# Performance work log

Measured on AMD Instinct MI355X. Metric: run time of the kernel, lower is better.

The kernel has to match this reference:

```python
import jax, jax.numpy as jnp
import numpy as np

B, T, CH, Hs, Ws = 2, 64, 512, 24, 24
DIM = CH // 2          # 256, attention channel dim
HEADS = 8
HEAD_DIM = DIM // HEADS  # 32
MAX_SEQ = 64


def setup_inputs() -> dict:
    key = jax.random.key(0)
    ks = jax.random.split(key, 6)
    return {
        "x": jax.random.normal(ks[0], (B, T, CH, Hs, Ws), dtype=jnp.float32),
        "rpb_table": jax.random.normal(ks[1], (2 * MAX_SEQ - 1, HEADS), dtype=jnp.float32) * 0.02,
        "qkv_w": jax.random.normal(ks[2], (3 * DIM, DIM), dtype=jnp.float32) * 0.02,
        "qkv_b": jax.random.normal(ks[3], (3 * DIM,), dtype=jnp.float32) * 0.02,
        "proj_w": jax.random.normal(ks[4], (DIM, DIM), dtype=jnp.float32) * 0.02,
        "proj_b": jax.random.normal(ks[5], (DIM,), dtype=jnp.float32) * 0.02,
    }


def reference(x, rpb_table, qkv_w, qkv_b, proj_w, proj_b):
    b, t, c, h, w = x.shape
    half = c // 2
    a_part = x[:, :, :half]       # (B,T,half,H,W) untouched branch
    b_part = x[:, :, half:]       # attention branch

    # 'b t c h w -> (b h w) t c'
    xb = jnp.transpose(b_part, (0, 3, 4, 1, 2)).reshape(b * h * w, t, half)
    B_, N, C = xb.shape
    scale = HEAD_DIM ** -0.5

    qkv = xb @ qkv_w.T + qkv_b                        # (B_, N, 3*C)
    qkv = qkv.reshape(B_, N, 3, HEADS, HEAD_DIM)
    qkv = jnp.transpose(qkv, (2, 0, 3, 1, 4))          # (3, B_, heads, N, hd)
    q, k, v = qkv[0] * scale, qkv[1], qkv[2]

    attn = jnp.einsum('bhnd,bhmd->bhnm', q, k)         # (B_, heads, N, N)

    # relative position bias: index = p2 - p1 + (MAX_SEQ - 1)
    pos = jnp.arange(t)
    rel_idx = pos[None, :] - pos[:, None] + (MAX_SEQ - 1)   # (N, N)
    bias = rpb_table[rel_idx]                              # (N, N, heads)
    bias = jnp.transpose(bias, (2, 0, 1))                  # (heads, N, N)
    attn = attn + bias[None]

    # causal (mask_future=True): -inf strictly above the diagonal
    causal = jnp.where(pos[None, :] > pos[:, None], -jnp.inf, 0.0).astype(attn.dtype)
    attn = attn + causal[None, None]

    attn = jax.nn.softmax(attn, axis=-1)

    out = jnp.einsum('bhnm,bhmd->bhnd', attn, v)       # (B_, heads, N, hd)
    out = jnp.transpose(out, (0, 2, 1, 3)).reshape(B_, N, C)
    out = out @ proj_w.T + proj_b

    # '(b h w) t c -> b t c h w'
    out = out.reshape(b, h, w, t, half)
    out = jnp.transpose(out, (0, 3, 4, 1, 2))

    return jnp.concatenate([a_part, out], axis=2)
```

## Files before the change

### kernel.cpp

```cpp
#include <hip/hip_runtime.h>
#include <hip/hip_bf16.h>

typedef __attribute__((ext_vector_type(4))) float  f32x4;
typedef __attribute__((ext_vector_type(8))) short  bf16x8;
typedef __attribute__((ext_vector_type(8))) unsigned short u16x8;
typedef __attribute__((ext_vector_type(4))) unsigned short u16x4;

__device__ __forceinline__ unsigned short f2bf(float f) {
    union { float f; unsigned u; } v; v.f = f;
    unsigned u = v.u;
    unsigned r = u + 0x7fffu + ((u >> 16) & 1u);
    return (unsigned short)(r >> 16);
}

__device__ __forceinline__ void gload16(const void* g, void* l) {
    __builtin_amdgcn_global_load_lds((const __attribute__((address_space(1))) unsigned*)g,
                                     (__attribute__((address_space(3))) unsigned*)l, 16, 0, 0);
}


__global__ void cvt_weights(const float* __restrict__ qkv_w, const float* __restrict__ proj_w,
                            unsigned short* __restrict__ wq, unsigned short* __restrict__ wp) {
    int i = blockIdx.x * 256 + threadIdx.x;
    if (i < 196608) wq[i] = f2bf(qkv_w[i]);
    else            wp[i - 196608] = f2bf(proj_w[i - 196608]);
}

__global__ void copy_a(const float* __restrict__ x, float* __restrict__ out) {
    long long i = (long long)blockIdx.x * 256 + threadIdx.x;
    int chunk = (int)(i / 36864);
    int r     = (int)(i % 36864);
    size_t off = (size_t)chunk * 73728 + r;
    ((float4*)out)[off] = ((const float4*)x)[off];
}

__global__ __launch_bounds__(256) void transpose_b(const float* __restrict__ x,
                                                   unsigned short* __restrict__ xb) {
    __shared__ unsigned short tile[256][72];
    const int bt  = blockIdx.x;
    const int hw0 = blockIdx.y * 64;
    const int tid = threadIdx.x;
    const float* src = x + ((size_t)bt * 512 + 256) * 576 + hw0;
    const int c_sub = tid >> 4, l16 = tid & 15;
    #pragma unroll
    for (int it = 0; it < 16; ++it) {
        int cc = it * 16 + c_sub;
        const float4 v = *(const float4*)(src + (size_t)cc * 576 + l16 * 4);
        tile[cc][l16 * 4 + 0] = f2bf(v.x);
        tile[cc][l16 * 4 + 1] = f2bf(v.y);
        tile[cc][l16 * 4 + 2] = f2bf(v.z);
        tile[cc][l16 * 4 + 3] = f2bf(v.w);
    }
    __syncthreads();
    const int row = tid >> 2;
    const int cs  = (tid & 3) * 64;
    const int b = bt >> 6, t = bt & 63;
    size_t m = (size_t)t * 1152 + (size_t)b * 576 + hw0 + row;
    unsigned short* dst = xb + m * 256 + cs;
    #pragma unroll
    for (int q = 0; q < 8; ++q) {
        u16x8 v;
        #pragma unroll
        for (int u = 0; u < 8; ++u) v[u] = tile[cs + q * 8 + u][row];
        *(u16x8*)(dst + q * 8) = v;
    }
}

__global__ __launch_bounds__(256, 4) void gemm_qkv(const unsigned short* __restrict__ A,
                                                   const unsigned short* __restrict__ Wt,
                                                   const float* __restrict__ bias,
                                                   unsigned short* __restrict__ out) {
    __shared__ unsigned short Ws[128 * 64];
    __shared__ unsigned short Xs[128 * 64];
    const int m0 = blockIdx.x * 128, n0 = blockIdx.y * 128;
    const int tid = threadIdx.x;
    const int lane = tid & 63, w = tid >> 6;
    const int wy = w >> 1, wx = w & 1;
    const int c = lane & 15, g = lane >> 4;
    const int lr = lane >> 3, lu = lane & 7;
    const int su = lu ^ lr;
    const int cs7 = c & 7;
    f32x4 acc[4][4] = {};
    for (int k0 = 0; k0 < 256; k0 += 64) {
        #pragma unroll
        for (int q = 0; q < 4; ++q) {
            int R = w * 32 + q * 8;
            gload16(Wt + (size_t)(n0 + R + lr) * 256 + k0 + su * 8, &Ws[R * 64]);
            gload16(A  + (size_t)(m0 + R + lr) * 256 + k0 + su * 8, &Xs[R * 64]);
        }
        __syncthreads();
        #pragma unroll
        for (int kk = 0; kk < 2; ++kk) {
            bf16x8 af[4], bx[4];
            #pragma unroll
            for (int a2 = 0; a2 < 4; ++a2)
                af[a2] = *(const bf16x8*)(&Ws[(wy * 64 + a2 * 16 + c) * 64 + (((kk * 4 + g) ^ cs7) * 8)]);
            #pragma unroll
            for (int b2 = 0; b2 < 4; ++b2)
                bx[b2] = *(const bf16x8*)(&Xs[(wx * 64 + b2 * 16 + c) * 64 + (((kk * 4 + g) ^ cs7) * 8)]);
            #pragma unroll
            for (int a2 = 0; a2 < 4; ++a2)
                #pragma unroll
                for (int b2 = 0; b2 < 4; ++b2)
                    acc[a2][b2] = __builtin_amdgcn_mfma_f32_16x16x32_bf16(af[a2], bx[b2], acc[a2][b2], 0, 0, 0);
        }
        __syncthreads();
    }
    #pragma unroll
    for (int a2 = 0; a2 < 4; ++a2) {
        int n = n0 + wy * 64 + a2 * 16 + g * 4;
        float4 bv = *(const float4*)(bias + n);
        #pragma unroll
        for (int b2 = 0; b2 < 4; ++b2) {
            int m = m0 + wx * 64 + b2 * 16 + c;
            u16x4 v;
            v[0] = f2bf(acc[a2][b2][0] + bv.x);
            v[1] = f2bf(acc[a2][b2][1] + bv.y);
            v[2] = f2bf(acc[a2][b2][2] + bv.z);
            v[3] = f2bf(acc[a2][b2][3] + bv.w);
            *(u16x4*)(out + (size_t)m * 768 + n) = v;
        }
    }
}

__global__ __launch_bounds__(64) void attn_kernel(const unsigned short* __restrict__ qkv,
                                                  const float* __restrict__ rpb,
                                                  unsigned short* __restrict__ att) {
    __shared__ float bias_s[127];
    __shared__ unsigned short vT[32][72];
    __shared__ unsigned short P[64][72];
    const int blk = blockIdx.x;
    const int p = blk >> 3, h = blk & 7;
    const int lane = threadIdx.x;
    const int c = lane & 15, g = lane >> 4;

    bias_s[lane] = rpb[lane * 8 + h];
    if (lane < 63) bias_s[64 + lane] = rpb[(64 + lane) * 8 + h];

    {
        const unsigned short* vrow = qkv + (size_t)(lane * 1152 + p) * 768 + 512 + h * 32;
        #pragma unroll
        for (int q = 0; q < 4; ++q) {
            u16x8 v = *(const u16x8*)(vrow + q * 8);
            #pragma unroll
            for (int u = 0; u < 8; ++u) vT[q * 8 + u][lane] = v[u];
        }
    }
    bf16x8 qf[4], kf[4];
    #pragma unroll
    for (int mt = 0; mt < 4; ++mt)
        qf[mt] = *(const bf16x8*)(qkv + (size_t)((mt * 16 + c) * 1152 + p) * 768 + h * 32 + g * 8);
    #pragma unroll
    for (int nt = 0; nt < 4; ++nt)
        kf[nt] = *(const bf16x8*)(qkv + (size_t)((nt * 16 + c) * 1152 + p) * 768 + 256 + h * 32 + g * 8);
    f32x4 s[4][4] = {};
    #pragma unroll
    for (int mt = 0; mt < 4; ++mt)
        #pragma unroll
        for (int nt = 0; nt < 4; ++nt)
            s[mt][nt] = __builtin_amdgcn_mfma_f32_16x16x32_bf16(qf[mt], kf[nt], s[mt][nt], 0, 0, 0);
    __syncthreads();

    const float scale = 0.17677669529663687f;
    #pragma unroll
    for (int mt = 0; mt < 4; ++mt) {
        #pragma unroll
        for (int r = 0; r < 4; ++r) {
            int i = mt * 16 + g * 4 + r;
            float vals[4];
            #pragma unroll
            for (int nt = 0; nt < 4; ++nt) {
                int j = nt * 16 + c;
                float v = s[mt][nt][r] * scale + bias_s[j - i + 63];
                vals[nt] = (j > i) ? -1e30f : v;
            }
            float mx = fmaxf(fmaxf(vals[0], vals[1]), fmaxf(vals[2], vals[3]));
            #pragma unroll
            for (int off = 1; off < 16; off <<= 1) mx = fmaxf(mx, __shfl_xor(mx, off, 64));
            float sum = 0.f;
            #pragma unroll
            for (int nt = 0; nt < 4; ++nt) { vals[nt] = __expf(vals[nt] - mx); sum += vals[nt]; }
            #pragma unroll
            for (int off = 1; off < 16; off <<= 1) sum += __shfl_xor(sum, off, 64);
            float inv = 1.0f / sum;
            #pragma unroll
            for (int nt = 0; nt < 4; ++nt) P[i][nt * 16 + c] = f2bf(vals[nt] * inv);
        }
    }
    __syncthreads();

    f32x4 o[4][2] = {};
    #pragma unroll
    for (int kk = 0; kk < 2; ++kk) {
        bf16x8 pa[4], vb[2];
        #pragma unroll
        for (int mt = 0; mt < 4; ++mt)
            pa[mt] = *(const bf16x8*)(&P[mt * 16 + c][kk * 32 + g * 8]);
        #pragma unroll
        for (int nt = 0; nt < 2; ++nt)
            vb[nt] = *(const bf16x8*)(&vT[nt * 16 + c][kk * 32 + g * 8]);
        #pragma unroll
        for (int mt = 0; mt < 4; ++mt)
            #pragma unroll
            for (int nt = 0; nt < 2; ++nt)
                o[mt][nt] = __builtin_amdgcn_mfma_f32_16x16x32_bf16(pa[mt], vb[nt], o[mt][nt], 0, 0, 0);
    }
    #pragma unroll
    for (int mt = 0; mt < 4; ++mt)
        #pragma unroll
        for (int nt = 0; nt < 2; ++nt) {
            int d = nt * 16 + c;
            #pragma unroll
            for (int r = 0; r < 4; ++r) {
                int i = mt * 16 + g * 4 + r;
                att[(size_t)(i * 1152 + p) * 256 + h * 32 + d] = f2bf(o[mt][nt][r]);
            }
        }
}

__global__ __launch_bounds__(256, 4) void gemm_proj(const unsigned short* __restrict__ A,
                                                    const unsigned short* __restrict__ Wt,
                                                    const float* __restrict__ bias,
                                                    float* __restrict__ out) {
    __shared__ unsigned short Ws[128 * 64];
    __shared__ unsigned short Xs[128 * 64];
    const int m0 = blockIdx.x * 128, n0 = blockIdx.y * 128;
    const int tid = threadIdx.x;
    const int lane = tid & 63, w = tid >> 6;
    const int wy = w >> 1, wx = w & 1;
    const int c = lane & 15, g = lane >> 4;
    const int lr = lane >> 3, lu = lane & 7;
    const int su = lu ^ lr;
    const int cs7 = c & 7;
    f32x4 acc[4][4] = {};
    for (int k0 = 0; k0 < 256; k0 += 64) {
        #pragma unroll
        for (int q = 0; q < 4; ++q) {
            int R = w * 32 + q * 8;
            gload16(Wt + (size_t)(n0 + R + lr) * 256 + k0 + su * 8, &Ws[R * 64]);
            gload16(A  + (size_t)(m0 + R + lr) * 256 + k0 + su * 8, &Xs[R * 64]);
        }
        __syncthreads();
        #pragma unroll
        for (int kk = 0; kk < 2; ++kk) {
            bf16x8 af[4], bx[4];
            #pragma unroll
            for (int a2 = 0; a2 < 4; ++a2)
                af[a2] = *(const bf16x8*)(&Ws[(wy * 64 + a2 * 16 + c) * 64 + (((kk * 4 + g) ^ cs7) * 8)]);
            #pragma unroll
            for (int b2 = 0; b2 < 4; ++b2)
                bx[b2] = *(const bf16x8*)(&Xs[(wx * 64 + b2 * 16 + c) * 64 + (((kk * 4 + g) ^ cs7) * 8)]);
            #pragma unroll
            for (int a2 = 0; a2 < 4; ++a2)
                #pragma unroll
                for (int b2 = 0; b2 < 4; ++b2)
                    acc[a2][b2] = __builtin_amdgcn_mfma_f32_16x16x32_bf16(af[a2], bx[b2], acc[a2][b2], 0, 0, 0);
        }
        __syncthreads();
    }
    #pragma unroll
    for (int a2 = 0; a2 < 4; ++a2) {
        int n = n0 + wy * 64 + a2 * 16 + g * 4;
        float4 bv = *(const float4*)(bias + n);
        #pragma unroll
        for (int b2 = 0; b2 < 4; ++b2) {
            int m = m0 + wx * 64 + b2 * 16 + c;
            int t   = m / 1152;
            int rem = m % 1152;
            int bb  = rem / 576;
            int hw  = rem % 576;
            float* dst = out + ((size_t)(bb * 64 + t) * 512 + 256 + n) * 576 + hw;
            dst[0]        = acc[a2][b2][0] + bv.x;
            dst[576]      = acc[a2][b2][1] + bv.y;
            dst[2 * 576]  = acc[a2][b2][2] + bv.z;
            dst[3 * 576]  = acc[a2][b2][3] + bv.w;
        }
    }
}

extern "C" void kernel_launch(void* const* d_in, const int* in_sizes, int n_in,
                              void* d_out, int out_size, void* d_ws, size_t ws_size,
                              hipStream_t stream) {
    (void)in_sizes; (void)n_in; (void)out_size;
    const float* x      = (const float*)d_in[0];
    const float* rpb    = (const float*)d_in[1];
    const float* qkv_w  = (const float*)d_in[2];
    const float* qkv_b  = (const float*)d_in[3];
    const float* proj_w = (const float*)d_in[4];
    const float* proj_b = (const float*)d_in[5];
    float* out = (float*)d_out;

    char* ws = (char*)d_ws;
    unsigned short* wq  = (unsigned short*)ws;
    unsigned short* wp  = (unsigned short*)(ws + 393216);
    unsigned short* xb  = (unsigned short*)(ws + 524288);
    unsigned short* qkv = (unsigned short*)(ws + 524288 + 37748736);
    unsigned short* att = xb;
    if (ws_size < (size_t)524288 + 37748736 + 113246208) return;

    cvt_weights<<<1024, 256, 0, stream>>>(qkv_w, proj_w, wq, wp);
    copy_a<<<18432, 256, 0, stream>>>(x, out);
    transpose_b<<<dim3(128, 9), 256, 0, stream>>>(x, xb);
    gemm_qkv<<<dim3(576, 6), 256, 0, stream>>>(xb, wq, qkv_b, qkv);
    attn_kernel<<<9216, 64, 0, stream>>>(qkv, rpb, att);
    gemm_proj<<<dim3(576, 2), 256, 0, stream>>>(att, wp, proj_b, out);
}
```

Baseline: 225.8 us.

## Fuse QKV GEMM, attention, and projection into one per-sequence kernel

Measured after the change: 275.0 us. 21.8% more time.

```diff
diff --git a/kernel.cpp b/kernel.cpp
--- a/kernel.cpp
+++ b/kernel.cpp
@@ -55,7 +55,7 @@
     const int row = tid >> 2;
     const int cs  = (tid & 3) * 64;
     const int b = bt >> 6, t = bt & 63;
-    size_t m = (size_t)t * 1152 + (size_t)b * 576 + hw0 + row;
+    size_t m = ((size_t)(b * 576 + hw0 + row)) * 64 + t;
     unsigned short* dst = xb + m * 256 + cs;
     #pragma unroll
     for (int q = 0; q < 8; ++q) {
@@ -66,102 +66,103 @@
     }
 }
 
-__global__ __launch_bounds__(256, 4) void gemm_qkv(const unsigned short* __restrict__ A,
-                                                   const unsigned short* __restrict__ Wt,
-                                                   const float* __restrict__ bias,
-                                                   unsigned short* __restrict__ out) {
-    __shared__ unsigned short Ws[128 * 64];
-    __shared__ unsigned short Xs[128 * 64];
-    const int m0 = blockIdx.x * 128, n0 = blockIdx.y * 128;
-    const int tid = threadIdx.x;
+__global__ __launch_bounds__(512, 2) void fused_block(
+    const unsigned short* __restrict__ xb,
+    const unsigned short* __restrict__ wqkv,
+    const unsigned short* __restrict__ wproj,
+    const float* __restrict__ qkv_b,
+    const float* __restrict__ proj_b,
+    const float* __restrict__ rpb,
+    float* __restrict__ out)
+{
+    __shared__ unsigned short xs[16384];
+    __shared__ unsigned short wbuf[8][7424];
+    __shared__ float bias_s[1016];
+
+    const int tid  = threadIdx.x;
     const int lane = tid & 63, w = tid >> 6;
-    const int wy = w >> 1, wx = w & 1;
     const int c = lane & 15, g = lane >> 4;
-    const int lr = lane >> 3, lu = lane & 7;
-    const int su = lu ^ lr;
-    const int cs7 = c & 7;
-    f32x4 acc[4][4] = {};
-    for (int k0 = 0; k0 < 256; k0 += 64) {
-        #pragma unroll
-        for (int q = 0; q < 4; ++q) {
-            int R = w * 32 + q * 8;
-            gload16(Wt + (size_t)(n0 + R + lr) * 256 + k0 + su * 8, &Ws[R * 64]);
-            gload16(A  + (size_t)(m0 + R + lr) * 256 + k0 + su * 8, &Xs[R * 64]);
-        }
-        __syncthreads();
-        #pragma unroll
-        for (int kk = 0; kk < 2; ++kk) {
-            bf16x8 af[4], bx[4];
-            #pragma unroll
-            for (int a2 = 0; a2 < 4; ++a2)
-                af[a2] = *(const bf16x8*)(&Ws[(wy * 64 + a2 * 16 + c) * 64 + (((kk * 4 + g) ^ cs7) * 8)]);
+    const int c7 = c & 7;
+    const int bid = blockIdx.x;
+    const int p  = (bid & 7) * 144 + (bid >> 3);
+    const int b  = p / 576, hw = p % 576;
+
+    const unsigned short* src = xb + (size_t)p * 16384;
+    #pragma unroll
+    for (int it = 0; it < 4; ++it) {
+        int U = it * 512 + tid;
+        int r = U >> 5, u = U & 31;
+        gload16(src + r * 256 + ((u ^ (r & 7)) << 3), &xs[U << 3]);
+    }
+    if (tid < 1016) bias_s[tid] = rpb[tid];
+    __syncthreads();
+
+    unsigned short* Q  = &wbuf[w][0];
+    unsigned short* Kl = &wbuf[w][2560];
+    unsigned short* Vt = &wbuf[w][5120];
+    unsigned short* P  = &wbuf[w][0];
+
+    {
+        f32x4 acc[3][2][4] = {};
+        #pragma unroll
+        for (int ks = 0; ks < 8; ++ks) {
+            bf16x8 bx[4];
             #pragma unroll
             for (int b2 = 0; b2 < 4; ++b2)
-                bx[b2] = *(const bf16x8*)(&Xs[(wx * 64 + b2 * 16 + c) * 64 + (((kk * 4 + g) ^ cs7) * 8)]);
-            #pragma unroll
-            for (int a2 = 0; a2 < 4; ++a2)
+                bx[b2] = *(const bf16x8*)(&xs[(b2 * 16 + c) * 256 + (((ks * 4 + g) ^ c7) << 3)]);
+            #pragma unroll
+            for (int mat = 0; mat < 3; ++mat) {
+                bf16x8 af[2];
                 #pragma unroll
-                for (int b2 = 0; b2 < 4; ++b2)
-                    acc[a2][b2] = __builtin_amdgcn_mfma_f32_16x16x32_bf16(af[a2], bx[b2], acc[a2][b2], 0, 0, 0);
-        }
-        __syncthreads();
-    }
-    #pragma unroll
-    for (int a2 = 0; a2 < 4; ++a2) {
-        int n = n0 + wy * 64 + a2 * 16 + g * 4;
-        float4 bv = *(const float4*)(bias + n);
-        #pragma unroll
-        for (int b2 = 0; b2 < 4; ++b2) {
-            int m = m0 + wx * 64 + b2 * 16 + c;
-            u16x4 v;
-            v[0] = f2bf(acc[a2][b2][0] + bv.x);
-            v[1] = f2bf(acc[a2][b2][1] + bv.y);
-            v[2] = f2bf(acc[a2][b2][2] + bv.z);
-            v[3] = f2bf(acc[a2][b2][3] + bv.w);
-            *(u16x4*)(out + (size_t)m * 768 + n) = v;
-        }
-    }
-}
-
-__global__ __launch_bounds__(64) void attn_kernel(const unsigned short* __restrict__ qkv,
-                                                  const float* __restrict__ rpb,
-                                                  unsigned short* __restrict__ att) {
-    __shared__ float bias_s[127];
-    __shared__ unsigned short vT[32][72];
-    __shared__ unsigned short P[64][72];
-    const int blk = blockIdx.x;
-    const int p = blk >> 3, h = blk & 7;
-    const int lane = threadIdx.x;
-    const int c = lane & 15, g = lane >> 4;
-
-    bias_s[lane] = rpb[lane * 8 + h];
-    if (lane < 63) bias_s[64 + lane] = rpb[(64 + lane) * 8 + h];
-
-    {
-        const unsigned short* vrow = qkv + (size_t)(lane * 1152 + p) * 768 + 512 + h * 32;
-        #pragma unroll
-        for (int q = 0; q < 4; ++q) {
-            u16x8 v = *(const u16x8*)(vrow + q * 8);
-            #pragma unroll
-            for (int u = 0; u < 8; ++u) vT[q * 8 + u][lane] = v[u];
-        }
-    }
+                for (int a2 = 0; a2 < 2; ++a2)
+                    af[a2] = *(const bf16x8*)(wqkv + (size_t)(mat * 256 + w * 32 + a2 * 16 + c) * 256 + ks * 32 + g * 8);
+                #pragma unroll
+                for (int a2 = 0; a2 < 2; ++a2)
+                    #pragma unroll
+                    for (int b2 = 0; b2 < 4; ++b2)
+                        acc[mat][a2][b2] = __builtin_amdgcn_mfma_f32_16x16x32_bf16(af[a2], bx[b2], acc[mat][a2][b2], 0, 0, 0);
+            }
+        }
+        const float scale = 0.17677669529663687f;
+        #pragma unroll
+        for (int a2 = 0; a2 < 2; ++a2) {
+            float4 bq = *(const float4*)(qkv_b +       w * 32 + a2 * 16 + g * 4);
+            float4 bk = *(const float4*)(qkv_b + 256 + w * 32 + a2 * 16 + g * 4);
+            float4 bv = *(const float4*)(qkv_b + 512 + w * 32 + a2 * 16 + g * 4);
+            #pragma unroll
+            for (int b2 = 0; b2 < 4; ++b2) {
+                int t = b2 * 16 + c;
+                u16x4 vq, vk;
+                vq[0] = f2bf((acc[0][a2][b2][0] + bq.x) * scale);
+                vq[1] = f2bf((acc[0][a2][b2][1] + bq.y) * scale);
+                vq[2] = f2bf((acc[0][a2][b2][2] + bq.z) * scale);
+                vq[3] = f2bf((acc[0][a2][b2][3] + bq.w) * scale);
+                *(u16x4*)(&Q[t * 40 + a2 * 16 + g * 4]) = vq;
+                vk[0] = f2bf(acc[1][a2][b2][0] + bk.x);
+                vk[1] = f2bf(acc[1][a2][b2][1] + bk.y);
+                vk[2] = f2bf(acc[1][a2][b2][2] + bk.z);
+                vk[3] = f2bf(acc[1][a2][b2][3] + bk.w);
+                *(u16x4*)(&Kl[t * 40 + a2 * 16 + g * 4]) = vk;
+                Vt[(a2 * 16 + g * 4 + 0) * 72 + t] = f2bf(acc[2][a2][b2][0] + bv.x);
+                Vt[(a2 * 16 + g * 4 + 1) * 72 + t] = f2bf(acc[2][a2][b2][1] + bv.y);
+                Vt[(a2 * 16 + g * 4 + 2) * 72 + t] = f2bf(acc[2][a2][b2][2] + bv.z);
+                Vt[(a2 * 16 + g * 4 + 3) * 72 + t] = f2bf(acc[2][a2][b2][3] + bv.w);
+            }
+        }
+    }
+
     bf16x8 qf[4], kf[4];
     #pragma unroll
+    for (int mt = 0; mt < 4; ++mt) qf[mt] = *(const bf16x8*)(&Q[(mt * 16 + c) * 40 + g * 8]);
+    #pragma unroll
+    for (int nt = 0; nt < 4; ++nt) kf[nt] = *(const bf16x8*)(&Kl[(nt * 16 + c) * 40 + g * 8]);
+    f32x4 S[4][4] = {};
+    #pragma unroll
     for (int mt = 0; mt < 4; ++mt)
-        qf[mt] = *(const bf16x8*)(qkv + (size_t)((mt * 16 + c) * 1152 + p) * 768 + h * 32 + g * 8);
-    #pragma unroll
-    for (int nt = 0; nt < 4; ++nt)
-        kf[nt] = *(const bf16x8*)(qkv + (size_t)((nt * 16 + c) * 1152 + p) * 768 + 256 + h * 32 + g * 8);
-    f32x4 s[4][4] = {};
-    #pragma unroll
-    for (int mt = 0; mt < 4; ++mt)
         #pragma unroll
         for (int nt = 0; nt < 4; ++nt)
-            s[mt][nt] = __builtin_amdgcn_mfma_f32_16x16x32_bf16(qf[mt], kf[nt], s[mt][nt], 0, 0, 0);
-    __syncthreads();
-
-    const float scale = 0.17677669529663687f;
+            S[mt][nt] = __builtin_amdgcn_mfma_f32_16x16x32_bf16(qf[mt], kf[nt], S[mt][nt], 0, 0, 0);
+
     #pragma unroll
     for (int mt = 0; mt < 4; ++mt) {
         #pragma unroll
@@ -171,7 +172,7 @@
             #pragma unroll
             for (int nt = 0; nt < 4; ++nt) {
                 int j = nt * 16 + c;
-                float v = s[mt][nt][r] * scale + bias_s[j - i + 63];
+                float v = S[mt][nt][r] + bias_s[(j - i + 63) * 8 + w];
                 vals[nt] = (j > i) ? -1e30f : v;
             }
             float mx = fmaxf(fmaxf(vals[0], vals[1]), fmaxf(vals[2], vals[3]));
@@ -184,96 +185,68 @@
             for (int off = 1; off < 16; off <<= 1) sum += __shfl_xor(sum, off, 64);
             float inv = 1.0f / sum;
             #pragma unroll
-            for (int nt = 0; nt < 4; ++nt) P[i][nt * 16 + c] = f2bf(vals[nt] * inv);
-        }
-    }
-    __syncthreads();
-
-    f32x4 o[4][2] = {};
+            for (int nt = 0; nt < 4; ++nt) P[i * 72 + nt * 16 + c] = f2bf(vals[nt] * inv);
+        }
+    }
+
+    f32x4 O[4][2] = {};
     #pragma unroll
     for (int kk = 0; kk < 2; ++kk) {
         bf16x8 pa[4], vb[2];
         #pragma unroll
         for (int mt = 0; mt < 4; ++mt)
-            pa[mt] = *(const bf16x8*)(&P[mt * 16 + c][kk * 32 + g * 8]);
+            pa[mt] = *(const bf16x8*)(&P[(mt * 16 + c) * 72 + kk * 32 + g * 8]);
         #pragma unroll
         for (int nt = 0; nt < 2; ++nt)
-            vb[nt] = *(const bf16x8*)(&vT[nt * 16 + c][kk * 32 + g * 8]);
+            vb[nt] = *(const bf16x8*)(&Vt[(nt * 16 + c) * 72 + kk * 32 + g * 8]);
         #pragma unroll
         for (int mt = 0; mt < 4; ++mt)
             #pragma unroll
             for (int nt = 0; nt < 2; ++nt)
-                o[mt][nt] = __builtin_amdgcn_mfma_f32_16x16x32_bf16(pa[mt], vb[nt], o[mt][nt], 0, 0, 0);
-    }
+                O[mt][nt] = __builtin_amdgcn_mfma_f32_16x16x32_bf16(pa[mt], vb[nt], O[mt][nt], 0, 0, 0);
+    }
+
+    __syncthreads();
     #pragma unroll
     for (int mt = 0; mt < 4; ++mt)
         #pragma unroll
-        for (int nt = 0; nt < 2; ++nt) {
-            int d = nt * 16 + c;
+        for (int nt = 0; nt < 2; ++nt)
             #pragma unroll
             for (int r = 0; r < 4; ++r) {
-                int i = mt * 16 + g * 4 + r;
-                att[(size_t)(i * 1152 + p) * 256 + h * 32 + d] = f2bf(o[mt][nt][r]);
-            }
-        }
-}
-
-__global__ __launch_bounds__(256, 4) void gemm_proj(const unsigned short* __restrict__ A,
-                                                    const unsigned short* __restrict__ Wt,
-                                                    const float* __restrict__ bias,
-                                                    float* __restrict__ out) {
-    __shared__ unsigned short Ws[128 * 64];
-    __shared__ unsigned short Xs[128 * 64];
-    const int m0 = blockIdx.x * 128, n0 = blockIdx.y * 128;
-    const int tid = threadIdx.x;
-    const int lane = tid & 63, w = tid >> 6;
-    const int wy = w >> 1, wx = w & 1;
-    const int c = lane & 15, g = lane >> 4;
-    const int lr = lane >> 3, lu = lane & 7;
-    const int su = lu ^ lr;
-    const int cs7 = c & 7;
-    f32x4 acc[4][4] = {};
-    for (int k0 = 0; k0 < 256; k0 += 64) {
-        #pragma unroll
-        for (int q = 0; q < 4; ++q) {
-            int R = w * 32 + q * 8;
-            gload16(Wt + (size_t)(n0 + R + lr) * 256 + k0 + su * 8, &Ws[R * 64]);
-            gload16(A  + (size_t)(m0 + R + lr) * 256 + k0 + su * 8, &Xs[R * 64]);
-        }
-        __syncthreads();
-        #pragma unroll
-        for (int kk = 0; kk < 2; ++kk) {
-            bf16x8 af[4], bx[4];
-            #pragma unroll
-            for (int a2 = 0; a2 < 4; ++a2)
-                af[a2] = *(const bf16x8*)(&Ws[(wy * 64 + a2 * 16 + c) * 64 + (((kk * 4 + g) ^ cs7) * 8)]);
+                int t  = mt * 16 + g * 4 + r;
+                int cg = w * 32 + nt * 16 + c;
+                xs[t * 256 + (((cg >> 3) ^ (t & 7)) << 3) + (cg & 7)] = f2bf(O[mt][nt][r]);
+            }
+    __syncthreads();
+
+    f32x4 ap[2][4] = {};
+    #pragma unroll
+    for (int ks = 0; ks < 8; ++ks) {
+        bf16x8 af[2], bx[4];
+        #pragma unroll
+        for (int a2 = 0; a2 < 2; ++a2)
+            af[a2] = *(const bf16x8*)(wproj + (size_t)(w * 32 + a2 * 16 + c) * 256 + ks * 32 + g * 8);
+        #pragma unroll
+        for (int b2 = 0; b2 < 4; ++b2)
+            bx[b2] = *(const bf16x8*)(&xs[(b2 * 16 + c) * 256 + (((ks * 4 + g) ^ c7) << 3)]);
+        #pragma unroll
+        for (int a2 = 0; a2 < 2; ++a2)
             #pragma unroll
             for (int b2 = 0; b2 < 4; ++b2)
-                bx[b2] = *(const bf16x8*)(&Xs[(wx * 64 + b2 * 16 + c) * 64 + (((kk * 4 + g) ^ cs7) * 8)]);
-            #pragma unroll
-            for (int a2 = 0; a2 < 4; ++a2)
-                #pragma unroll
-                for (int b2 = 0; b2 < 4; ++b2)
-                    acc[a2][b2] = __builtin_amdgcn_mfma_f32_16x16x32_bf16(af[a2], bx[b2], acc[a2][b2], 0, 0, 0);
-        }
-        __syncthreads();
-    }
-    #pragma unroll
-    for (int a2 = 0; a2 < 4; ++a2) {
-        int n = n0 + wy * 64 + a2 * 16 + g * 4;
-        float4 bv = *(const float4*)(bias + n);
+                ap[a2][b2] = __builtin_amdgcn_mfma_f32_16x16x32_bf16(af[a2], bx[b2], ap[a2][b2], 0, 0, 0);
+    }
+    #pragma unroll
+    for (int a2 = 0; a2 < 2; ++a2) {
+        int n = w * 32 + a2 * 16 + g * 4;
+        float4 pb = *(const float4*)(proj_b + n);
         #pragma unroll
         for (int b2 = 0; b2 < 4; ++b2) {
-            int m = m0 + wx * 64 + b2 * 16 + c;
-            int t   = m / 1152;
-            int rem = m % 1152;
-            int bb  = rem / 576;
-            int hw  = rem % 576;
-            float* dst = out + ((size_t)(bb * 64 + t) * 512 + 256 + n) * 576 + hw;
-            dst[0]        = acc[a2][b2][0] + bv.x;
-            dst[576]      = acc[a2][b2][1] + bv.y;
-            dst[2 * 576]  = acc[a2][b2][2] + bv.z;
-            dst[3 * 576]  = acc[a2][b2][3] + bv.w;
+            int t = b2 * 16 + c;
+            float* dst = out + ((size_t)((b * 64 + t) * 512 + 256 + n)) * 576 + hw;
+            dst[0]        = ap[a2][b2][0] + pb.x;
+            dst[576]      = ap[a2][b2][1] + pb.y;
+            dst[2 * 576]  = ap[a2][b2][2] + pb.z;
+            dst[3 * 576]  = ap[a2][b2][3] + pb.w;
         }
     }
 }
@@ -291,17 +264,13 @@
     float* out = (float*)d_out;
 
     char* ws = (char*)d_ws;
-    unsigned short* wq  = (unsigned short*)ws;
-    unsigned short* wp  = (unsigned short*)(ws + 393216);
-    unsigned short* xb  = (unsigned short*)(ws + 524288);
-    unsigned short* qkv = (unsigned short*)(ws + 524288 + 37748736);
-    unsigned short* att = xb;
-    if (ws_size < (size_t)524288 + 37748736 + 113246208) return;
+    unsigned short* wq = (unsigned short*)ws;
+    unsigned short* wp = (unsigned short*)(ws + 393216);
+    unsigned short* xb = (unsigned short*)(ws + 524288);
+    if (ws_size < (size_t)524288 + 37748736) return;
 
     cvt_weights<<<1024, 256, 0, stream>>>(qkv_w, proj_w, wq, wp);
     copy_a<<<18432, 256, 0, stream>>>(x, out);
     transpose_b<<<dim3(128, 9), 256, 0, stream>>>(x, xb);
-    gemm_qkv<<<dim3(576, 6), 256, 0, stream>>>(xb, wq, qkv_b, qkv);
-    attn_kernel<<<9216, 64, 0, stream>>>(qkv, rpb, att);
-    gemm_proj<<<dim3(576, 2), 256, 0, stream>>>(att, wp, proj_b, out);
-}
+    fused_block<<<1152, 512, 0, stream>>>(xb, wq, wp, qkv_b, proj_b, rpb, out);
+}
```
